# Kernel tuning notes

Hardware: AMD Instinct MI355X
Metric: run time of the kernel (lower is better)

The kernel has to match this reference:

```python
import jax, jax.numpy as jnp
import numpy as np

B, T, D_OBS, D, N, H = 256, 64, 512, 128, 16, 256  # H = max(2*D, D_OBS//2)
NUM_ITERS = 3
ALPHA = 0.7  # temporal_alpha


def _ln(x, g, b, eps=1e-5):
    mu = x.mean(-1, keepdims=True)
    var = ((x - mu) ** 2).mean(-1, keepdims=True)
    return (x - mu) / jnp.sqrt(var + eps) * g + b


def setup_inputs() -> dict:
    key = jax.random.key(0)
    ks = jax.random.split(key, 16)
    def p(i, shape, s=0.05):
        return jax.random.normal(ks[i], shape, jnp.float32) * s
    return {
        "observations": jax.random.normal(ks[0], (B, T, D_OBS), jnp.float32),
        "enc_W1": p(1, (D_OBS, H)), "enc_b1": jnp.zeros((H,), jnp.float32),
        "enc_W2": p(2, (H, D)), "enc_b2": jnp.zeros((D,), jnp.float32),
        "skip_W": p(3, (D_OBS, D)),
        "slot_mu": p(4, (1, N, D)),
        "Wk": p(5, (D, D)), "Wv": p(6, (D, D)), "Wq": p(7, (D, D)),
        "gru_Wih": p(8, (D, 3 * D)), "gru_Whh": p(9, (D, 3 * D)),
        "gru_bih": jnp.zeros((3 * D,), jnp.float32), "gru_bhh": jnp.zeros((3 * D,), jnp.float32),
        "mlp_W1": p(10, (D, D)), "mlp_b1": jnp.zeros((D,), jnp.float32),
        "mlp_W2": p(11, (D, D)), "mlp_b2": jnp.zeros((D,), jnp.float32),
        "ln_in_g": jnp.ones((D,), jnp.float32), "ln_in_b": jnp.zeros((D,), jnp.float32),
        "ln_sl_g": jnp.ones((D,), jnp.float32), "ln_sl_b": jnp.zeros((D,), jnp.float32),
        "ln_mlp_g": jnp.ones((D,), jnp.float32), "ln_mlp_b": jnp.zeros((D,), jnp.float32),
        "Wt": p(12, (D, D)),
    }


def reference(observations, enc_W1, enc_b1, enc_W2, enc_b2, skip_W, slot_mu,
              Wk, Wv, Wq, gru_Wih, gru_Whh, gru_bih, gru_bhh,
              mlp_W1, mlp_b1, mlp_W2, mlp_b2,
              ln_in_g, ln_in_b, ln_sl_g, ln_sl_b, ln_mlp_g, ln_mlp_b, Wt):
    Bt = observations.shape[0]
    scale = jnp.sqrt(jnp.asarray(D, jnp.float32))

    def gru(x, h):  # torch GRUCell math; gates ordered (r, z, n)
        gi = x @ gru_Wih + gru_bih
        gh = h @ gru_Whh + gru_bhh
        ir, iz, inn = jnp.split(gi, 3, -1)
        hr, hz, hn = jnp.split(gh, 3, -1)
        r = jax.nn.sigmoid(ir + hr)
        zg = jax.nn.sigmoid(iz + hz)
        n = jnp.tanh(inn + r * hn)
        return (1.0 - zg) * n + zg * h

    def slot_attention(z):  # z: (B, D) -> slots (B, N, D); eval mode (no noise)
        inp = _ln(z, ln_in_g, ln_in_b)
        k = inp @ Wk  # (B, D)
        v = inp @ Wv  # (B, D)
        slots = jnp.broadcast_to(slot_mu, (Bt, N, D))
        for _ in range(NUM_ITERS):
            q = _ln(slots, ln_sl_g, ln_sl_b) @ Wq  # (B, N, D)
            logits = jnp.einsum('bnd,bd->bn', q, k) / scale
            attn = jax.nn.softmax(logits, axis=1)  # competition over slots
            updates = attn[..., None] * v[:, None, :]  # (B, N, D)
            slots = gru(updates, slots)
            sm = _ln(slots, ln_mlp_g, ln_mlp_b)
            slots = slots + (jax.nn.relu(sm @ mlp_W1 + mlp_b1) @ mlp_W2 + mlp_b2)
        nrm = jnp.linalg.norm(slots, axis=-1, keepdims=True)
        return slots / jnp.maximum(nrm, 1e-8)  # F.normalize

    def encode(obs_t):  # (B, D_obs) -> (B, D)
        h = jax.nn.gelu(obs_t @ enc_W1 + enc_b1, approximate=False)
        return jnp.tanh(h @ enc_W2 + enc_b2 + obs_t @ skip_W)

    slots0 = slot_attention(encode(observations[:, 0]))  # t=0: no temporal blend

    def step(prev_slots, obs_t):
        slots = slot_attention(encode(obs_t))
        temporal = jnp.tanh(prev_slots @ Wt)
        slots = ALPHA * slots + (1.0 - ALPHA) * temporal
        return slots, slots

    obs_rest = jnp.swapaxes(observations[:, 1:], 0, 1)  # (T-1, B, D_obs)
    _, rest = jax.lax.scan(step, slots0, obs_rest)  # (T-1, B, N, D)
    latent = jnp.concatenate([slots0[:, None], jnp.swapaxes(rest, 0, 1)], axis=1)
    return latent  # (B, T, N, D)
```

## Files before the change

kernel.cpp:

```cpp
#include <hip/hip_runtime.h>
#include <math.h>

#define B_ 256
#define T_ 64
#define DOBS 512
#define D_ 128
#define N_ 16
#define H_ 256

typedef unsigned short u16;
typedef short bf16x8 __attribute__((ext_vector_type(8)));
typedef float f32x4 __attribute__((ext_vector_type(4)));

union FragU { bf16x8 v; uint4 u; };

#define MFMA(ACC, A, Bv) (ACC) = __builtin_amdgcn_mfma_f32_16x16x32_bf16((A), (Bv), (ACC), 0, 0, 0)
#define MFMA2(ACC, AH, AL, Bv) do { MFMA(ACC, AH, Bv); MFMA(ACC, AL, Bv); } while (0)

#define OFF_EW1T   0
#define OFF_EW2T   131072
#define OFF_SKIPT  163840
#define OFF_WKVT   229376
#define OFF_WQT    262144
#define OFF_WIHT   278528
#define OFF_WHHT   327680
#define OFF_MW1T   376832
#define OFF_MW2T   393216
#define OFF_WTT    409600

__device__ __forceinline__ unsigned rne16(float f) {
    unsigned u = __float_as_uint(f);
    return (u + 0x7FFFu + ((u >> 16) & 1u)) >> 16;
}
__device__ __forceinline__ float fromhi(unsigned h) { return __uint_as_float(h << 16); }
__device__ __forceinline__ u16 f2b(float f) { return (u16)rne16(f); }
__device__ __forceinline__ float sigmoidf_(float x) { return 1.0f / (1.0f + expf(-x)); }

__device__ __forceinline__ void mk_pack(const float* x, FragU& fh, FragU& fl) {
    unsigned h[8], l[8];
#pragma unroll
    for (int j = 0; j < 8; ++j) {
        h[j] = rne16(x[j]);
        l[j] = rne16(x[j] - fromhi(h[j]));
    }
    fh.u = make_uint4(h[0] | (h[1] << 16), h[2] | (h[3] << 16), h[4] | (h[5] << 16), h[6] | (h[7] << 16));
    fl.u = make_uint4(l[0] | (l[1] << 16), l[2] | (l[3] << 16), l[4] | (l[5] << 16), l[6] | (l[7] << 16));
}

__device__ __forceinline__ void mk_raw(const float* p, FragU& fh, FragU& fl) {
    float4 a = *(const float4*)p, b = *(const float4*)(p + 4);
    float x[8] = {a.x, a.y, a.z, a.w, b.x, b.y, b.z, b.w};
    mk_pack(x, fh, fl);
}

__device__ __forceinline__ void mk_aff(const float* p, float mu, float rs,
                                       const float* gp, const float* bp,
                                       FragU& fh, FragU& fl) {
    float4 a = *(const float4*)p, b = *(const float4*)(p + 4);
    float4 g0 = *(const float4*)gp, g1 = *(const float4*)(gp + 4);
    float4 b0 = *(const float4*)bp, b1 = *(const float4*)(bp + 4);
    float x[8];
    x[0] = (a.x - mu) * rs * g0.x + b0.x;  x[1] = (a.y - mu) * rs * g0.y + b0.y;
    x[2] = (a.z - mu) * rs * g0.z + b0.z;  x[3] = (a.w - mu) * rs * g0.w + b0.w;
    x[4] = (b.x - mu) * rs * g1.x + b1.x;  x[5] = (b.y - mu) * rs * g1.y + b1.y;
    x[6] = (b.z - mu) * rs * g1.z + b1.z;  x[7] = (b.w - mu) * rs * g1.w + b1.w;
    mk_pack(x, fh, fl);
}

__device__ __forceinline__ void mk_scaled(const float* p, float sc, FragU& fh, FragU& fl) {
    float4 a = *(const float4*)p, b = *(const float4*)(p + 4);
    float x[8] = {sc * a.x, sc * a.y, sc * a.z, sc * a.w, sc * b.x, sc * b.y, sc * b.z, sc * b.w};
    mk_pack(x, fh, fl);
}

__global__ __launch_bounds__(256) void prep_kernel(
    const float* __restrict__ eW1, const float* __restrict__ eW2, const float* __restrict__ skipW,
    const float* __restrict__ Wk, const float* __restrict__ Wv, const float* __restrict__ Wq,
    const float* __restrict__ Wih, const float* __restrict__ Whh,
    const float* __restrict__ mW1, const float* __restrict__ mW2, const float* __restrict__ Wt,
    u16* __restrict__ ws)
{
    int id = blockIdx.y;
    const float* src; int dstoff, logk, N;
    switch (id) {
        case 0:  src = eW1;   dstoff = OFF_EW1T;  logk = 9; N = 256; break;
        case 1:  src = eW2;   dstoff = OFF_EW2T;  logk = 8; N = 128; break;
        case 2:  src = skipW; dstoff = OFF_SKIPT; logk = 9; N = 128; break;
        case 3:  src = Wk;    dstoff = OFF_WKVT;  logk = 7; N = 128; break;
        case 4:  src = Wv;    dstoff = OFF_WKVT + 16384; logk = 7; N = 128; break;
        case 5:  src = Wq;    dstoff = OFF_WQT;   logk = 7; N = 128; break;
        case 6:  src = Wih;   dstoff = OFF_WIHT;  logk = 7; N = 384; break;
        case 7:  src = Whh;   dstoff = OFF_WHHT;  logk = 7; N = 384; break;
        case 8:  src = mW1;   dstoff = OFF_MW1T;  logk = 7; N = 128; break;
        case 9:  src = mW2;   dstoff = OFF_MW2T;  logk = 7; N = 128; break;
        default: src = Wt;    dstoff = OFF_WTT;   logk = 7; N = 128; break;
    }
    int idx = blockIdx.x * 256 + threadIdx.x;
    int K = 1 << logk;
    if (idx < K * N) {
        int n = idx >> logk, k = idx & (K - 1);
        ws[dstoff + idx] = f2b(src[k * N + n]);
    }
}

__global__ __launch_bounds__(256) void sa2_kernel(
    const float* __restrict__ obs,
    const float* __restrict__ eb1, const float* __restrict__ eb2,
    const float* __restrict__ slot_mu,
    const float* __restrict__ bih, const float* __restrict__ bhh,
    const float* __restrict__ mb1, const float* __restrict__ mb2,
    const float* __restrict__ g_in, const float* __restrict__ be_in,
    const float* __restrict__ g_sl, const float* __restrict__ be_sl,
    const float* __restrict__ g_ml, const float* __restrict__ be_ml,
    const u16* __restrict__ ws, float* __restrict__ out)
{
    __shared__ __align__(16) float slots_s[64 * 132];
    __shared__ __align__(16) float scratch[4352];
    __shared__ __align__(16) float k_s[4 * 132];
    __shared__ __align__(16) float v_s[4 * 132];
    __shared__ __align__(16) float par_s[6 * 128];
    __shared__ __align__(16) float bias_s[512];
    __shared__ __align__(16) float gv_s[4 * 392];
    __shared__ float rs_s[64];
    __shared__ float logit_s[64];
    __shared__ float zmu_s[4], zrs_s[4];

    float* obs_s = scratch;
    float* h_s   = scratch + 2064;
    float* z_s   = scratch + 3104;
    u16*   hid_s = (u16*)scratch;

    const int tid = threadIdx.x;
    const int wave = tid >> 6, lane = tid & 63;
    const int l15 = lane & 15, quad = lane >> 4;
    const int r0 = blockIdx.x * 4;

    if (tid < 128) {
        par_s[tid]       = g_in[tid];  par_s[128 + tid] = be_in[tid];
        par_s[256 + tid] = g_sl[tid];  par_s[384 + tid] = be_sl[tid];
        par_s[512 + tid] = g_ml[tid];  par_s[640 + tid] = be_ml[tid];
        bias_s[256 + tid] = bih[256 + tid];
        bias_s[384 + tid] = bhh[256 + tid];
    }
    if (tid < 256) bias_s[tid] = bih[tid] + bhh[tid];
    for (int i4 = tid; i4 < 512; i4 += 256) {
        int g2 = i4 >> 7, c4 = i4 & 127;
        *((float4*)(obs_s + g2 * 516) + c4) = *((const float4*)(obs + (size_t)(r0 + g2) * 512) + c4);
    }
    __syncthreads();

    {
        f32x4 acc[4] = {{0}, {0}, {0}, {0}};
        const float* abase = obs_s + (l15 & 3) * 516;
#pragma unroll 1
        for (int ks = 0; ks < 16; ++ks) {
            FragU ah, al;
            mk_raw(abase + ks * 32 + quad * 8, ah, al);
#pragma unroll
            for (int tt = 0; tt < 4; ++tt) {
                int row = (wave * 4 + tt) * 16 + l15;
                FragU b; b.u = *(const uint4*)(ws + OFF_EW1T + row * 512 + ks * 32 + quad * 8);
                MFMA2(acc[tt], ah.v, al.v, b.v);
            }
        }
        {
            f32x4 av = acc[0];
            if (quad == 1) av = acc[1];
            if (quad == 2) av = acc[2];
            if (quad == 3) av = acc[3];
            int col = (wave * 4 + quad) * 16 + l15;
            float bb = eb1[col];
#pragma unroll
            for (int reg = 0; reg < 4; ++reg) {
                float x = av[reg] + bb;
                h_s[reg * 260 + col] = 0.5f * x * (1.0f + erff(x * 0.7071067811865475f));
            }
        }
    }
    __syncthreads();

    {
        f32x4 acc[2] = {{0}, {0}};
        const float* hbase = h_s + (l15 & 3) * 260;
#pragma unroll 1
        for (int ks = 0; ks < 8; ++ks) {
            FragU ah, al;
            mk_raw(hbase + ks * 32 + quad * 8, ah, al);
#pragma unroll
            for (int tt = 0; tt < 2; ++tt) {
                int row = (wave * 2 + tt) * 16 + l15;
                FragU b; b.u = *(const uint4*)(ws + OFF_EW2T + row * 256 + ks * 32 + quad * 8);
                MFMA2(acc[tt], ah.v, al.v, b.v);
            }
        }
        const float* obase = obs_s + (l15 & 3) * 516;
#pragma unroll 1
        for (int ks = 0; ks < 16; ++ks) {
            FragU ah, al;
            mk_raw(obase + ks * 32 + quad * 8, ah, al);
#pragma unroll
            for (int tt = 0; tt < 2; ++tt) {
                int row = (wave * 2 + tt) * 16 + l15;
                FragU b; b.u = *(const uint4*)(ws + OFF_SKIPT + row * 512 + ks * 32 + quad * 8);
                MFMA2(acc[tt], ah.v, al.v, b.v);
            }
        }
        if (quad < 2) {
            f32x4 av = (quad == 0) ? acc[0] : acc[1];
            int col = (wave * 2 + quad) * 16 + l15;
            float bb = eb2[col];
#pragma unroll
            for (int reg = 0; reg < 4; ++reg)
                z_s[reg * 132 + col] = tanhf(av[reg] + bb);
        }
    }
    __syncthreads();

    {
        const float* row = z_s + wave * 132;
        float x0 = row[lane], x1 = row[64 + lane];
        float s = x0 + x1;
        s += __shfl_xor(s, 1);  s += __shfl_xor(s, 2);  s += __shfl_xor(s, 4);
        s += __shfl_xor(s, 8);  s += __shfl_xor(s, 16); s += __shfl_xor(s, 32);
        float mu = s * (1.0f / 128.0f);
        float d0 = x0 - mu, d1 = x1 - mu;
        float v = fmaf(d0, d0, d1 * d1);
        v += __shfl_xor(v, 1);  v += __shfl_xor(v, 2);  v += __shfl_xor(v, 4);
        v += __shfl_xor(v, 8);  v += __shfl_xor(v, 16); v += __shfl_xor(v, 32);
        if (lane == 0) { zmu_s[wave] = mu; zrs_s[wave] = rsqrtf(v * (1.0f / 128.0f) + 1e-5f); }
    }
    __syncthreads();

    {
        f32x4 acc[4] = {{0}, {0}, {0}, {0}};
        const float* zbase = z_s + (l15 & 3) * 132;
        float zmu = zmu_s[l15 & 3], zrs = zrs_s[l15 & 3];
#pragma unroll 1
        for (int ks = 0; ks < 4; ++ks) {
            FragU ah, al;
            mk_aff(zbase + ks * 32 + quad * 8, zmu, zrs,
                   par_s + ks * 32 + quad * 8, par_s + 128 + ks * 32 + quad * 8, ah, al);
#pragma unroll
            for (int tt = 0; tt < 4; ++tt) {
                int row = (wave * 4 + tt) * 16 + l15;
                FragU b; b.u = *(const uint4*)(ws + OFF_WKVT + row * 128 + ks * 32 + quad * 8);
                MFMA2(acc[tt], ah.v, al.v, b.v);
            }
        }
        {
            f32x4 av = acc[0];
            if (quad == 1) av = acc[1];
            if (quad == 2) av = acc[2];
            if (quad == 3) av = acc[3];
            int col = (wave * 4 + quad) * 16 + l15;
#pragma unroll
            for (int reg = 0; reg < 4; ++reg) {
                if (col < 128) k_s[reg * 132 + col] = av[reg];
                else           v_s[reg * 132 + col - 128] = av[reg];
            }
        }
    }
    __syncthreads();

    {
        f32x4 ag[6] = {{0}, {0}, {0}, {0}, {0}, {0}};
        const float* vbase = v_s + (l15 & 3) * 132;
#pragma unroll 1
        for (int ks = 0; ks < 4; ++ks) {
            FragU ah, al;
            mk_raw(vbase + ks * 32 + quad * 8, ah, al);
#pragma unroll
            for (int tt = 0; tt < 6; ++tt) {
                int row = (wave * 6 + tt) * 16 + l15;
                FragU b; b.u = *(const uint4*)(ws + OFF_WIHT + row * 128 + ks * 32 + quad * 8);
                MFMA2(ag[tt], ah.v, al.v, b.v);
            }
        }
#pragma unroll
        for (int tt = 0; tt < 6; ++tt) {
            if ((tt & 3) == quad) {
                int col = (wave * 6 + tt) * 16 + l15;
#pragma unroll
                for (int reg = 0; reg < 4; ++reg)
                    gv_s[reg * 392 + col] = ag[tt][reg];
            }
        }
    }
    __syncthreads();

    const int g = wave;
    const int srow0 = g * 16;
    for (int i4 = lane; i4 < 512; i4 += 64) {
        int row = i4 >> 5, c4 = i4 & 31;
        *((float4*)(slots_s + (srow0 + row) * 132) + c4) = *((const float4*)slot_mu + i4);
    }
    const float* gvrow = gv_s + g * 392;

    for (int iter = 0; iter < 3; ++iter) {
        float myMu, myRs;
        {
            const float* rowp = slots_s + (srow0 + l15) * 132;
            float s0 = 0, s1 = 0, s2 = 0, s3 = 0;
#pragma unroll
            for (int j = 0; j < 8; ++j) {
                s0 += rowp[quad + 16 * j];
                s1 += rowp[quad + 16 * j + 4];
                s2 += rowp[quad + 16 * j + 8];
                s3 += rowp[quad + 16 * j + 12];
            }
            float s = (s0 + s1) + (s2 + s3);
            s += __shfl_xor(s, 16); s += __shfl_xor(s, 32);
            myMu = s * (1.0f / 128.0f);
            float v0 = 0, v1 = 0, v2 = 0, v3 = 0;
#pragma unroll
            for (int j = 0; j < 8; ++j) {
                float d0 = rowp[quad + 16 * j] - myMu;      v0 = fmaf(d0, d0, v0);
                float d1 = rowp[quad + 16 * j + 4] - myMu;  v1 = fmaf(d1, d1, v1);
                float d2 = rowp[quad + 16 * j + 8] - myMu;  v2 = fmaf(d2, d2, v2);
                float d3 = rowp[quad + 16 * j + 12] - myMu; v3 = fmaf(d3, d3, v3);
            }
            float v = (v0 + v1) + (v2 + v3);
            v += __shfl_xor(v, 16); v += __shfl_xor(v, 32);
            myRs = rsqrtf(v * (1.0f / 128.0f) + 1e-5f);
        }

        {
            FragU ah[4], al[4];
#pragma unroll
            for (int ks = 0; ks < 4; ++ks)
                mk_aff(slots_s + (srow0 + l15) * 132 + ks * 32 + quad * 8, myMu, myRs,
                       par_s + 256 + ks * 32 + quad * 8, par_s + 384 + ks * 32 + quad * 8,
                       ah[ks], al[ks]);
            float lp[4] = {0, 0, 0, 0};
#pragma unroll 1
            for (int t = 0; t < 8; ++t) {
                f32x4 a = {0};
#pragma unroll
                for (int ks = 0; ks < 4; ++ks) {
                    FragU b; b.u = *(const uint4*)(ws + OFF_WQT + (t * 16 + l15) * 128 + ks * 32 + quad * 8);
                    MFMA2(a, ah[ks].v, al[ks].v, b.v);
                }
                float kc = k_s[g * 132 + t * 16 + l15];
#pragma unroll
                for (int reg = 0; reg < 4; ++reg) lp[reg] = fmaf(a[reg], kc, lp[reg]);
            }
#pragma unroll
            for (int reg = 0; reg < 4; ++reg) {
                lp[reg] += __shfl_xor(lp[reg], 1);
                lp[reg] += __shfl_xor(lp[reg], 2);
                lp[reg] += __shfl_xor(lp[reg], 4);
                lp[reg] += __shfl_xor(lp[reg], 8);
            }
            if (l15 == 0) {
#pragma unroll
                for (int reg = 0; reg < 4; ++reg)
                    logit_s[srow0 + quad * 4 + reg] = lp[reg] * 0.08838834764831845f;
            }
        }

        float attn_me;
        {
            float x = logit_s[srow0 + l15];
            float mx = fmaxf(x, __shfl_xor(x, 1));
            mx = fmaxf(mx, __shfl_xor(mx, 2));
            mx = fmaxf(mx, __shfl_xor(mx, 4));
            mx = fmaxf(mx, __shfl_xor(mx, 8));
            float e = expf(x - mx);
            float den = e;
            den += __shfl_xor(den, 1);
            den += __shfl_xor(den, 2);
            den += __shfl_xor(den, 4);
            den += __shfl_xor(den, 8);
            attn_me = e / den;
        }

        {
            float attn_r[4];
#pragma unroll
            for (int reg = 0; reg < 4; ++reg) attn_r[reg] = __shfl(attn_me, quad * 4 + reg);
            FragU ash[4], asl[4];
#pragma unroll
            for (int ks = 0; ks < 4; ++ks)
                mk_raw(slots_s + (srow0 + l15) * 132 + ks * 32 + quad * 8, ash[ks], asl[ks]);
#pragma unroll 1
            for (int cg = 0; cg < 8; ++cg) {
                f32x4 ar = {0}, az = {0}, anh = {0};
                const int rowb = cg * 16 + l15;
#pragma unroll
                for (int ks = 0; ks < 4; ++ks) {
                    const int koff = ks * 32 + quad * 8;
                    FragU b;
                    b.u = *(const uint4*)(ws + OFF_WHHT + rowb * 128 + koff);
                    MFMA2(ar, ash[ks].v, asl[ks].v, b.v);
                    b.u = *(const uint4*)(ws + OFF_WHHT + (128 + rowb) * 128 + koff);
                    MFMA2(az, ash[ks].v, asl[ks].v, b.v);
                    b.u = *(const uint4*)(ws + OFF_WHHT + (256 + rowb) * 128 + koff);
                    MFMA2(anh, ash[ks].v, asl[ks].v, b.v);
                }
                const int cc = cg * 16 + l15;
                float gvr = gvrow[cc], gvz = gvrow[128 + cc], gvn = gvrow[256 + cc];
#pragma unroll
                for (int reg = 0; reg < 4; ++reg) {
                    int row = srow0 + quad * 4 + reg;
                    float a = attn_r[reg];
                    float rg = sigmoidf_(fmaf(a, gvr, ar[reg] + bias_s[cc]));
                    float zg = sigmoidf_(fmaf(a, gvz, az[reg] + bias_s[128 + cc]));
                    float ng = tanhf(fmaf(a, gvn, bias_s[256 + cc]) + rg * (anh[reg] + bias_s[384 + cc]));
                    float hp = slots_s[row * 132 + cc];
                    slots_s[row * 132 + cc] = (1.0f - zg) * ng + zg * hp;
                }
            }
        }

        {
            const float* rowp = slots_s + (srow0 + l15) * 132;
            float s0 = 0, s1 = 0, s2 = 0, s3 = 0;
#pragma unroll
            for (int j = 0; j < 8; ++j) {
                s0 += rowp[quad + 16 * j];
                s1 += rowp[quad + 16 * j + 4];
                s2 += rowp[quad + 16 * j + 8];
                s3 += rowp[quad + 16 * j + 12];
            }
            float s = (s0 + s1) + (s2 + s3);
            s += __shfl_xor(s, 16); s += __shfl_xor(s, 32);
            float mu2 = s * (1.0f / 128.0f);
            float v0 = 0, v1 = 0, v2 = 0, v3 = 0;
#pragma unroll
            for (int j = 0; j < 8; ++j) {
                float d0 = rowp[quad + 16 * j] - mu2;      v0 = fmaf(d0, d0, v0);
                float d1 = rowp[quad + 16 * j + 4] - mu2;  v1 = fmaf(d1, d1, v1);
                float d2 = rowp[quad + 16 * j + 8] - mu2;  v2 = fmaf(d2, d2, v2);
                float d3 = rowp[quad + 16 * j + 12] - mu2; v3 = fmaf(d3, d3, v3);
            }
            float v = (v0 + v1) + (v2 + v3);
            v += __shfl_xor(v, 16); v += __shfl_xor(v, 32);
            float rs2 = rsqrtf(v * (1.0f / 128.0f) + 1e-5f);

            FragU ah[4], al[4];
#pragma unroll
            for (int ks = 0; ks < 4; ++ks)
                mk_aff(rowp + ks * 32 + quad * 8, mu2, rs2,
                       par_s + 512 + ks * 32 + quad * 8, par_s + 640 + ks * 32 + quad * 8,
                       ah[ks], al[ks]);
#pragma unroll 1
            for (int t = 0; t < 8; ++t) {
                f32x4 a = {0};
#pragma unroll
                for (int ks = 0; ks < 4; ++ks) {
                    FragU b; b.u = *(const uint4*)(ws + OFF_MW1T + (t * 16 + l15) * 128 + ks * 32 + quad * 8);
                    MFMA2(a, ah[ks].v, al[ks].v, b.v);
                }
                int cc = t * 16 + l15;
                float bb = mb1[cc];
#pragma unroll
                for (int reg = 0; reg < 4; ++reg)
                    hid_s[(srow0 + quad * 4 + reg) * 136 + cc] = f2b(fmaxf(a[reg] + bb, 0.0f));
            }
        }
        {
            FragU hf[4];
#pragma unroll
            for (int ks = 0; ks < 4; ++ks)
                hf[ks].u = *(const uint4*)(hid_s + (srow0 + l15) * 136 + ks * 32 + quad * 8);
#pragma unroll 1
            for (int t = 0; t < 8; ++t) {
                f32x4 a = {0};
#pragma unroll
                for (int ks = 0; ks < 4; ++ks) {
                    FragU b; b.u = *(const uint4*)(ws + OFF_MW2T + (t * 16 + l15) * 128 + ks * 32 + quad * 8);
                    MFMA(a, hf[ks].v, b.v);
                }
                int cc = t * 16 + l15;
                float bb = mb2[cc];
#pragma unroll
                for (int reg = 0; reg < 4; ++reg)
                    slots_s[(srow0 + quad * 4 + reg) * 132 + cc] += a[reg] + bb;
            }
        }
    }

    {
        const float* rowp = slots_s + (srow0 + l15) * 132;
        float a0 = 0, a1 = 0, a2 = 0, a3 = 0;
#pragma unroll
        for (int j = 0; j < 8; ++j) {
            float x0 = rowp[quad + 16 * j];      a0 = fmaf(x0, x0, a0);
            float x1 = rowp[quad + 16 * j + 4];  a1 = fmaf(x1, x1, a1);
            float x2 = rowp[quad + 16 * j + 8];  a2 = fmaf(x2, x2, a2);
            float x3 = rowp[quad + 16 * j + 12]; a3 = fmaf(x3, x3, a3);
        }
        float ss = (a0 + a1) + (a2 + a3);
        ss += __shfl_xor(ss, 16); ss += __shfl_xor(ss, 32);
        if (quad == 0) rs_s[srow0 + l15] = 1.0f / fmaxf(sqrtf(ss), 1e-8f);
    }
    {
        size_t base = (size_t)(r0 + g) * 2048;
        for (int i4 = lane; i4 < 512; i4 += 64) {
            int row = i4 >> 5, c4 = i4 & 31;
            float4 vv = *((const float4*)(slots_s + (srow0 + row) * 132) + c4);
            float r = rs_s[srow0 + row];
            vv.x *= r; vv.y *= r; vv.z *= r; vv.w *= r;
            *((float4*)(out + base) + i4) = vv;
        }
    }
}

__global__ __launch_bounds__(64) void temporal2_kernel(
    const u16* __restrict__ ws, float* __restrict__ out)
{
    __shared__ __align__(16) u16 wt_s[128 * 136];
    __shared__ __align__(16) u16 prev_s[16 * 136];
    __shared__ __align__(16) float sa_s[16 * 132];

    const int lane = threadIdx.x;
    const int l15 = lane & 15, quad = lane >> 4;
    const int b = blockIdx.x;

    for (int idx = lane; idx < 2048; idx += 64) {
        int row = idx >> 4, ch = idx & 15;
        *(uint4*)(wt_s + row * 136 + ch * 8) = *(const uint4*)(ws + OFF_WTT + row * 128 + ch * 8);
    }
    {
        size_t base0 = (size_t)b * 64 * 2048;
        for (int i4 = lane; i4 < 512; i4 += 64) {
            float4 vv = *((const float4*)(out + base0) + i4);
            int row = i4 >> 5, c0 = (i4 & 31) * 4;
            ushort4 pk;
            pk.x = f2b(vv.x); pk.y = f2b(vv.y); pk.z = f2b(vv.z); pk.w = f2b(vv.w);
            *(ushort4*)(prev_s + row * 136 + c0) = pk;
        }
    }

    for (int t = 1; t < 64; ++t) {
        size_t base = ((size_t)b * 64 + t) * 2048;
        __syncthreads();
        FragU ap[4];
#pragma unroll
        for (int ks = 0; ks < 4; ++ks)
            ap[ks].u = *(const uint4*)(prev_s + l15 * 136 + ks * 32 + quad * 8);
        for (int i4 = lane; i4 < 512; i4 += 64) {
            float4 vv = *((const float4*)(out + base) + i4);
            *((float4*)(sa_s + (i4 >> 5) * 132) + (i4 & 31)) = vv;
        }
        f32x4 acc[8] = {{0}, {0}, {0}, {0}, {0}, {0}, {0}, {0}};
#pragma unroll
        for (int tt = 0; tt < 8; ++tt) {
#pragma unroll
            for (int ks = 0; ks < 4; ++ks) {
                FragU bv; bv.u = *(const uint4*)(wt_s + (tt * 16 + l15) * 136 + ks * 32 + quad * 8);
                MFMA(acc[tt], ap[ks].v, bv.v);
            }
        }
        __syncthreads();
#pragma unroll
        for (int tt = 0; tt < 8; ++tt) {
            int col = tt * 16 + l15;
#pragma unroll
            for (int reg = 0; reg < 4; ++reg) {
                int row = quad * 4 + reg;
                float bl = 0.7f * sa_s[row * 132 + col] + 0.3f * tanhf(acc[tt][reg]);
                out[base + row * 128 + col] = bl;
                prev_s[row * 136 + col] = f2b(bl);
            }
        }
    }
}

extern "C" void kernel_launch(void* const* d_in, const int* in_sizes, int n_in,
                              void* d_out, int out_size, void* d_ws, size_t ws_size,
                              hipStream_t stream) {
    const float* obs   = (const float*)d_in[0];
    const float* eW1   = (const float*)d_in[1];
    const float* eb1   = (const float*)d_in[2];
    const float* eW2   = (const float*)d_in[3];
    const float* eb2   = (const float*)d_in[4];
    const float* skipW = (const float*)d_in[5];
    const float* smu   = (const float*)d_in[6];
    const float* Wk    = (const float*)d_in[7];
    const float* Wv    = (const float*)d_in[8];
    const float* Wq    = (const float*)d_in[9];
    const float* Wih   = (const float*)d_in[10];
    const float* Whh   = (const float*)d_in[11];
    const float* bih   = (const float*)d_in[12];
    const float* bhh   = (const float*)d_in[13];
    const float* mW1   = (const float*)d_in[14];
    const float* mb1   = (const float*)d_in[15];
    const float* mW2   = (const float*)d_in[16];
    const float* mb2   = (const float*)d_in[17];
    const float* g_in  = (const float*)d_in[18];
    const float* be_in = (const float*)d_in[19];
    const float* g_sl  = (const float*)d_in[20];
    const float* be_sl = (const float*)d_in[21];
    const float* g_ml  = (const float*)d_in[22];
    const float* be_ml = (const float*)d_in[23];
    const float* Wt    = (const float*)d_in[24];
    float* out = (float*)d_out;
    u16* ws = (u16*)d_ws;

    prep_kernel<<<dim3(512, 11), 256, 0, stream>>>(eW1, eW2, skipW, Wk, Wv, Wq,
                                                   Wih, Whh, mW1, mW2, Wt, ws);
    sa2_kernel<<<B_ * T_ / 4, 256, 0, stream>>>(obs, eb1, eb2, smu, bih, bhh, mb1, mb2,
                                                g_in, be_in, g_sl, be_sl, g_ml, be_ml,
                                                ws, out);
    temporal2_kernel<<<B_, 64, 0, stream>>>(ws, out);
}
```

Before: 1.808 ms.

## Fold Wq into key vector to compute attention logits as dot products

Rewrites the logit as k·(LN(slot)@Wq), which equals LN(slot)·(Wq k). The folded vector Wq k, scaled by gamma, is precomputed once per row together with its sum and a bias term. Each iteration then needs only one fused pass over the slot row for mean, sum of squares and the dot product, replacing the per-iteration MFMA matmul with Wq. This adds a small fp32 matvec per block that reads Wq from global memory. The variance now uses a one-pass formula, which can lose some precision.

```diff
diff --git a/kernel.cpp b/kernel.cpp
--- a/kernel.cpp
+++ b/kernel.cpp
@@ -21,7 +21,6 @@
 #define OFF_EW2T   131072
 #define OFF_SKIPT  163840
 #define OFF_WKVT   229376
-#define OFF_WQT    262144
 #define OFF_WIHT   278528
 #define OFF_WHHT   327680
 #define OFF_MW1T   376832
@@ -67,15 +66,9 @@
     mk_pack(x, fh, fl);
 }
 
-__device__ __forceinline__ void mk_scaled(const float* p, float sc, FragU& fh, FragU& fl) {
-    float4 a = *(const float4*)p, b = *(const float4*)(p + 4);
-    float x[8] = {sc * a.x, sc * a.y, sc * a.z, sc * a.w, sc * b.x, sc * b.y, sc * b.z, sc * b.w};
-    mk_pack(x, fh, fl);
-}
-
 __global__ __launch_bounds__(256) void prep_kernel(
     const float* __restrict__ eW1, const float* __restrict__ eW2, const float* __restrict__ skipW,
-    const float* __restrict__ Wk, const float* __restrict__ Wv, const float* __restrict__ Wq,
+    const float* __restrict__ Wk, const float* __restrict__ Wv,
     const float* __restrict__ Wih, const float* __restrict__ Whh,
     const float* __restrict__ mW1, const float* __restrict__ mW2, const float* __restrict__ Wt,
     u16* __restrict__ ws)
@@ -88,11 +81,10 @@
         case 2:  src = skipW; dstoff = OFF_SKIPT; logk = 9; N = 128; break;
         case 3:  src = Wk;    dstoff = OFF_WKVT;  logk = 7; N = 128; break;
         case 4:  src = Wv;    dstoff = OFF_WKVT + 16384; logk = 7; N = 128; break;
-        case 5:  src = Wq;    dstoff = OFF_WQT;   logk = 7; N = 128; break;
-        case 6:  src = Wih;   dstoff = OFF_WIHT;  logk = 7; N = 384; break;
-        case 7:  src = Whh;   dstoff = OFF_WHHT;  logk = 7; N = 384; break;
-        case 8:  src = mW1;   dstoff = OFF_MW1T;  logk = 7; N = 128; break;
-        case 9:  src = mW2;   dstoff = OFF_MW2T;  logk = 7; N = 128; break;
+        case 5:  src = Wih;   dstoff = OFF_WIHT;  logk = 7; N = 384; break;
+        case 6:  src = Whh;   dstoff = OFF_WHHT;  logk = 7; N = 384; break;
+        case 7:  src = mW1;   dstoff = OFF_MW1T;  logk = 7; N = 128; break;
+        case 8:  src = mW2;   dstoff = OFF_MW2T;  logk = 7; N = 128; break;
         default: src = Wt;    dstoff = OFF_WTT;   logk = 7; N = 128; break;
     }
     int idx = blockIdx.x * 256 + threadIdx.x;
@@ -107,6 +99,7 @@
     const float* __restrict__ obs,
     const float* __restrict__ eb1, const float* __restrict__ eb2,
     const float* __restrict__ slot_mu,
+    const float* __restrict__ Wq,
     const float* __restrict__ bih, const float* __restrict__ bhh,
     const float* __restrict__ mb1, const float* __restrict__ mb2,
     const float* __restrict__ g_in, const float* __restrict__ be_in,
@@ -121,8 +114,9 @@
     __shared__ __align__(16) float par_s[6 * 128];
     __shared__ __align__(16) float bias_s[512];
     __shared__ __align__(16) float gv_s[4 * 392];
+    __shared__ __align__(16) float gkq_s[4 * 132];
+    __shared__ float sgkq_s[4], bkq_s[4];
     __shared__ float rs_s[64];
-    __shared__ float logit_s[64];
     __shared__ float zmu_s[4], zrs_s[4];
 
     float* obs_s = scratch;
@@ -262,6 +256,20 @@
     }
     __syncthreads();
 
+    for (int t5 = tid; t5 < 512; t5 += 256) {
+        int r = t5 >> 7, j = t5 & 127;
+        const float* krow = k_s + r * 132;
+        const float* wrow = Wq + j * 128;
+        float a0 = 0, a1 = 0, a2 = 0, a3 = 0;
+        for (int e = 0; e < 128; e += 4) {
+            float4 wv = *(const float4*)(wrow + e);
+            float4 kv = *(const float4*)(krow + e);
+            a0 = fmaf(wv.x, kv.x, a0); a1 = fmaf(wv.y, kv.y, a1);
+            a2 = fmaf(wv.z, kv.z, a2); a3 = fmaf(wv.w, kv.w, a3);
+        }
+        gkq_s[r * 132 + j] = (a0 + a1) + (a2 + a3);
+    }
+
     {
         f32x4 ag[6] = {{0}, {0}, {0}, {0}, {0}, {0}};
         const float* vbase = v_s + (l15 & 3) * 132;
@@ -285,6 +293,21 @@
                     gv_s[reg * 392 + col] = ag[tt][reg];
             }
         }
+    }
+    __syncthreads();
+
+    {
+        float* kqrow = gkq_s + wave * 132;
+        float k0 = kqrow[lane], k1 = kqrow[64 + lane];
+        float gk0 = par_s[256 + lane] * k0, gk1 = par_s[256 + 64 + lane] * k1;
+        float bk = par_s[384 + lane] * k0 + par_s[384 + 64 + lane] * k1;
+        float s = gk0 + gk1;
+        s += __shfl_xor(s, 1);  s += __shfl_xor(s, 2);  s += __shfl_xor(s, 4);
+        s += __shfl_xor(s, 8);  s += __shfl_xor(s, 16); s += __shfl_xor(s, 32);
+        bk += __shfl_xor(bk, 1);  bk += __shfl_xor(bk, 2);  bk += __shfl_xor(bk, 4);
+        bk += __shfl_xor(bk, 8);  bk += __shfl_xor(bk, 16); bk += __shfl_xor(bk, 32);
+        kqrow[lane] = gk0; kqrow[64 + lane] = gk1;
+        if (lane == 0) { sgkq_s[wave] = s; bkq_s[wave] = bk; }
     }
     __syncthreads();
 
@@ -294,78 +317,44 @@
         int row = i4 >> 5, c4 = i4 & 31;
         *((float4*)(slots_s + (srow0 + row) * 132) + c4) = *((const float4*)slot_mu + i4);
     }
+    const float sgkq = sgkq_s[g], bkq = bkq_s[g];
+    const float* gkrow = gkq_s + g * 132;
     const float* gvrow = gv_s + g * 392;
 
     for (int iter = 0; iter < 3; ++iter) {
-        float myMu, myRs;
+        float attn_me;
         {
             const float* rowp = slots_s + (srow0 + l15) * 132;
             float s0 = 0, s1 = 0, s2 = 0, s3 = 0;
+            float q0 = 0, q1 = 0, q2 = 0, q3 = 0;
+            float d0 = 0, d1 = 0, d2 = 0, d3 = 0;
 #pragma unroll
             for (int j = 0; j < 8; ++j) {
-                s0 += rowp[quad + 16 * j];
-                s1 += rowp[quad + 16 * j + 4];
-                s2 += rowp[quad + 16 * j + 8];
-                s3 += rowp[quad + 16 * j + 12];
-            }
-            float s = (s0 + s1) + (s2 + s3);
-            s += __shfl_xor(s, 16); s += __shfl_xor(s, 32);
-            myMu = s * (1.0f / 128.0f);
-            float v0 = 0, v1 = 0, v2 = 0, v3 = 0;
-#pragma unroll
-            for (int j = 0; j < 8; ++j) {
-                float d0 = rowp[quad + 16 * j] - myMu;      v0 = fmaf(d0, d0, v0);
-                float d1 = rowp[quad + 16 * j + 4] - myMu;  v1 = fmaf(d1, d1, v1);
-                float d2 = rowp[quad + 16 * j + 8] - myMu;  v2 = fmaf(d2, d2, v2);
-                float d3 = rowp[quad + 16 * j + 12] - myMu; v3 = fmaf(d3, d3, v3);
-            }
-            float v = (v0 + v1) + (v2 + v3);
-            v += __shfl_xor(v, 16); v += __shfl_xor(v, 32);
-            myRs = rsqrtf(v * (1.0f / 128.0f) + 1e-5f);
-        }
-
-        {
-            FragU ah[4], al[4];
-#pragma unroll
-            for (int ks = 0; ks < 4; ++ks)
-                mk_aff(slots_s + (srow0 + l15) * 132 + ks * 32 + quad * 8, myMu, myRs,
-                       par_s + 256 + ks * 32 + quad * 8, par_s + 384 + ks * 32 + quad * 8,
-                       ah[ks], al[ks]);
-            float lp[4] = {0, 0, 0, 0};
-#pragma unroll 1
-            for (int t = 0; t < 8; ++t) {
-                f32x4 a = {0};
-#pragma unroll
-                for (int ks = 0; ks < 4; ++ks) {
-                    FragU b; b.u = *(const uint4*)(ws + OFF_WQT + (t * 16 + l15) * 128 + ks * 32 + quad * 8);
-                    MFMA2(a, ah[ks].v, al[ks].v, b.v);
-                }
-                float kc = k_s[g * 132 + t * 16 + l15];
-#pragma unroll
-                for (int reg = 0; reg < 4; ++reg) lp[reg] = fmaf(a[reg], kc, lp[reg]);
-            }
-#pragma unroll
-            for (int reg = 0; reg < 4; ++reg) {
-                lp[reg] += __shfl_xor(lp[reg], 1);
-                lp[reg] += __shfl_xor(lp[reg], 2);
-                lp[reg] += __shfl_xor(lp[reg], 4);
-                lp[reg] += __shfl_xor(lp[reg], 8);
-            }
-            if (l15 == 0) {
-#pragma unroll
-                for (int reg = 0; reg < 4; ++reg)
-                    logit_s[srow0 + quad * 4 + reg] = lp[reg] * 0.08838834764831845f;
-            }
-        }
-
-        float attn_me;
-        {
-            float x = logit_s[srow0 + l15];
-            float mx = fmaxf(x, __shfl_xor(x, 1));
+                float x0 = rowp[quad + 16 * j],      gg0 = gkrow[quad + 16 * j];
+                float x1 = rowp[quad + 16 * j + 4],  gg1 = gkrow[quad + 16 * j + 4];
+                float x2 = rowp[quad + 16 * j + 8],  gg2 = gkrow[quad + 16 * j + 8];
+                float x3 = rowp[quad + 16 * j + 12], gg3 = gkrow[quad + 16 * j + 12];
+                s0 += x0; s1 += x1; s2 += x2; s3 += x3;
+                q0 = fmaf(x0, x0, q0); q1 = fmaf(x1, x1, q1);
+                q2 = fmaf(x2, x2, q2); q3 = fmaf(x3, x3, q3);
+                d0 = fmaf(x0, gg0, d0); d1 = fmaf(x1, gg1, d1);
+                d2 = fmaf(x2, gg2, d2); d3 = fmaf(x3, gg3, d3);
+            }
+            float s  = (s0 + s1) + (s2 + s3);
+            float qq = (q0 + q1) + (q2 + q3);
+            float dd = (d0 + d1) + (d2 + d3);
+            s  += __shfl_xor(s, 16);  s  += __shfl_xor(s, 32);
+            qq += __shfl_xor(qq, 16); qq += __shfl_xor(qq, 32);
+            dd += __shfl_xor(dd, 16); dd += __shfl_xor(dd, 32);
+            float mu = s * (1.0f / 128.0f);
+            float var = qq * (1.0f / 128.0f) - mu * mu;
+            float rs = rsqrtf(fmaxf(var, 0.0f) + 1e-5f);
+            float logit = (rs * (dd - mu * sgkq) + bkq) * 0.08838834764831845f;
+            float mx = fmaxf(logit, __shfl_xor(logit, 1));
             mx = fmaxf(mx, __shfl_xor(mx, 2));
             mx = fmaxf(mx, __shfl_xor(mx, 4));
             mx = fmaxf(mx, __shfl_xor(mx, 8));
-            float e = expf(x - mx);
+            float e = expf(logit - mx);
             float den = e;
             den += __shfl_xor(den, 1);
             den += __shfl_xor(den, 2);
@@ -598,9 +587,9 @@
     float* out = (float*)d_out;
     u16* ws = (u16*)d_ws;
 
-    prep_kernel<<<dim3(512, 11), 256, 0, stream>>>(eW1, eW2, skipW, Wk, Wv, Wq,
+    prep_kernel<<<dim3(512, 10), 256, 0, stream>>>(eW1, eW2, skipW, Wk, Wv,
                                                    Wih, Whh, mW1, mW2, Wt, ws);
-    sa2_kernel<<<B_ * T_ / 4, 256, 0, stream>>>(obs, eb1, eb2, smu, bih, bhh, mb1, mb2,
+    sa2_kernel<<<B_ * T_ / 4, 256, 0, stream>>>(obs, eb1, eb2, smu, Wq, bih, bhh, mb1, mb2,
                                                 g_in, be_in, g_sl, be_sl, g_ml, be_ml,
                                                 ws, out);
     temporal2_kernel<<<B_, 64, 0, stream>>>(ws, out);
```

Result: faster. 1.696 ms (-6.2%).
